# Kernel tuning notes

Hardware: AMD Instinct MI355X
Metric: run time of the kernel (lower is better)

The kernel has to match this reference:

```python
import jax, jax.numpy as jnp
import numpy as np
from jax import lax

DIM = 192
HEADS = 8
B, H, W = 8, 128, 128


def dwconv3x3(x, w):
    # x: [B,C,H,W], w: [C,1,3,3] depthwise (groups=C)
    return lax.conv_general_dilated(
        x, w, window_strides=(1, 1), padding='SAME',
        feature_group_count=x.shape[1],
        dimension_numbers=('NCHW', 'OIHW', 'NCHW'))


def conv1x1(x, w, b=None):
    # w: [Cout, Cin]
    y = jnp.einsum('oc,bchw->bohw', w, x)
    if b is not None:
        y = y + b[None, :, None, None]
    return y


def setup_inputs() -> dict:
    key = jax.random.key(0)
    ks = jax.random.split(key, 9)
    s = 0.02
    return {
        'x': jax.random.normal(ks[0], (B, DIM, H, W), jnp.float32),
        'w_qkv': jax.random.normal(ks[1], (3 * DIM, DIM), jnp.float32) * s,
        'b_qkv': jnp.zeros((3 * DIM,), jnp.float32),
        'w_dw': jax.random.normal(ks[2], (3 * DIM, 1, 3, 3), jnp.float32) * s,
        'b_dw': jnp.zeros((3 * DIM,), jnp.float32),
        'w_proj': jax.random.normal(ks[3], (DIM, DIM), jnp.float32) * s,
        'b_proj': jnp.zeros((DIM,), jnp.float32),
        'w_pos1': jax.random.normal(ks[4], (DIM, 1, 3, 3), jnp.float32) * s,
        'w_pos2': jax.random.normal(ks[5], (DIM, 1, 3, 3), jnp.float32) * s,
        'temperature': jnp.ones((HEADS, 1, 1), jnp.float32),
    }


def reference(x, w_qkv, b_qkv, w_dw, b_dw, w_proj, b_proj, w_pos1, w_pos2, temperature):
    b, c, h, w = x.shape
    heads = HEADS
    ch = c // heads

    qkv = conv1x1(x, w_qkv, b_qkv)
    qkv = dwconv3x3(qkv, w_dw) + b_dw[None, :, None, None]
    q_inp, k_inp, v_inp = jnp.split(qkv, 3, axis=1)

    def to_heads(t):  # [B,C,H,W] -> [B,heads,ch,HW]
        return t.reshape(b, heads, ch, h * w)

    q = to_heads(q_inp)
    k = to_heads(k_inp)
    v = to_heads(v_inp)

    # L2 normalize over hw (torch F.normalize, eps=1e-12)
    q = q / jnp.maximum(jnp.linalg.norm(q, axis=-1, keepdims=True), 1e-12)
    k = k / jnp.maximum(jnp.linalg.norm(k, axis=-1, keepdims=True), 1e-12)

    attn = jnp.einsum('bhce,bhde->bhcd', q, k) * temperature  # [B,heads,ch,ch]
    attn = jax.nn.softmax(attn, axis=-1)
    out = jnp.einsum('bhcd,bhde->bhce', attn, v)  # [B,heads,ch,HW]
    out = out.reshape(b, c, h, w)

    out = conv1x1(out, w_proj, b_proj)

    pos = dwconv3x3(v_inp, w_pos1)
    pos = jax.nn.gelu(pos, approximate=False)
    pos = dwconv3x3(pos, w_pos2)

    return out + pos
```

## Files before the change

### kernel.cpp

```cpp
#include <hip/hip_runtime.h>
#include <stdint.h>
#include <stddef.h>

#define NB 8
#define CC 192
#define C3 576
#define HGT 128
#define WID 128
#define HW 16384
#define NH 8
#define QKROW 49152

typedef short bf16x8 __attribute__((ext_vector_type(8)));
typedef float f32x4 __attribute__((ext_vector_type(4)));

__device__ __forceinline__ unsigned short f2bf(float f) {
  unsigned int u = __float_as_uint(f);
  u += 0x7fffu + ((u >> 16) & 1u);
  return (unsigned short)(u >> 16);
}
__device__ __forceinline__ float bf2f(unsigned short h) {
  return __uint_as_float(((unsigned int)h) << 16);
}
__device__ __forceinline__ float bflo(unsigned int v) {
  return __uint_as_float(v << 16);
}
__device__ __forceinline__ float bfhi(unsigned int v) {
  return __uint_as_float(v & 0xffff0000u);
}
__device__ __forceinline__ unsigned int pk2(float a, float b) {
  return (unsigned int)f2bf(a) | ((unsigned int)f2bf(b) << 16);
}
__device__ __forceinline__ void gl_lds16(const void* g, void* l) {
  __builtin_amdgcn_global_load_lds(
      (const __attribute__((address_space(1))) unsigned int*)(uintptr_t)g,
      (__attribute__((address_space(3))) unsigned int*)(uint32_t)(uintptr_t)l,
      16, 0, 0);
}
__device__ __forceinline__ int xcd_swz(int g, int n) {
  return (g & 7) * (n >> 3) + (g >> 3);
}

__global__ void kwprep(const float* __restrict__ wq, unsigned char* __restrict__ wb,
                       unsigned char* __restrict__ zero_region) {
  int f = blockIdx.x * 256 + threadIdx.x;
  if (f < 9984) *(uint4*)(zero_region + (size_t)f * 16) = (uint4){0, 0, 0, 0};
  if (f >= C3 * 24) return;
  int oc = f / 24, s = f % 24;
  unsigned int wv[4];
#pragma unroll
  for (int j = 0; j < 4; ++j)
    wv[j] = pk2(wq[oc * 192 + s * 8 + 2 * j], wq[oc * 192 + s * 8 + 2 * j + 1]);
  uint4 st; st.x = wv[0]; st.y = wv[1]; st.z = wv[2]; st.w = wv[3];
  *(uint4*)(wb + (size_t)oc * 384 + ((s ^ (oc & 7)) * 16)) = st;
}

__global__ __launch_bounds__(256) void kqkv(const float* __restrict__ x,
                                            const unsigned char* __restrict__ wb,
                                            const float* __restrict__ bqkv,
                                            unsigned short* __restrict__ vout,
                                            unsigned char* __restrict__ qkout) {
  __shared__ __align__(16) unsigned char lds[53248];
  const int ABF = 0;
  const int BB  = 24576;
  const int TR  = 49152;
  int wg = xcd_swz(blockIdx.x, gridDim.x);
  int t = wg & 255, b = wg >> 8;
  int p0 = t * 64;
  int tid = threadIdx.x;
  const unsigned char* gx = (const unsigned char*)(x + (size_t)b * CC * HW + p0);

  int p = tid & 63, sg = tid >> 6;
#pragma unroll
  for (int ck = 0; ck < 2; ++ck) {
#pragma unroll
    for (int i = 0; i < 6; ++i) {
      int f = i * 256 + tid;
      int ch = ck * 96 + (f >> 4), seg = f & 15;
      gl_lds16(gx + ((size_t)ch * HW + seg * 4) * 4, lds + BB + f * 16);
    }
    asm volatile("s_waitcnt vmcnt(0)" ::: "memory");
    __syncthreads();
    const float* lx = (const float*)(lds + BB);
#pragma unroll
    for (int s3 = 0; s3 < 3; ++s3) {
      int s = sg * 3 + s3;
      unsigned int wv[4];
#pragma unroll
      for (int j = 0; j < 4; ++j)
        wv[j] = pk2(lx[(s * 8 + 2 * j) * 64 + p], lx[(s * 8 + 2 * j + 1) * 64 + p]);
      uint4 st; st.x = wv[0]; st.y = wv[1]; st.z = wv[2]; st.w = wv[3];
      *(uint4*)(lds + ABF + ((ck * 12 + s) * 64 + p) * 16) = st;
    }
    __syncthreads();
  }
#pragma unroll
  for (int i = 0; i < 3; ++i)
    gl_lds16(wb + i * 4096 + tid * 16, lds + BB + i * 4096 + tid * 16);

  int lane = tid & 63, w = tid >> 6;
  int l15 = lane & 15, gq = lane >> 4;
  int pw = w * 16;
  int y = t >> 1, xh = (t & 1) * 8;
  int unitw = w * 2 + (gq >> 1);
  int sub8 = (gq & 1) * 8;
  int s4 = w * 4 + gq;
  int tc = tid & 31, tu = tid >> 5;
  int vcv = tid >> 3, vx = tid & 7;

  for (int j = 0; j < 18; ++j) {
    int ot = j >> 1, hh = j & 1, cur = j & 1;
    if (j == 0) { asm volatile("s_waitcnt vmcnt(0)" ::: "memory"); }
    else        { asm volatile("s_waitcnt vmcnt(1)" ::: "memory"); }
    __builtin_amdgcn_s_barrier();
    __builtin_amdgcn_sched_barrier(0);
    float bias0 = bqkv[ot * 64 + hh * 32 + l15];
    float bias1 = bqkv[ot * 64 + hh * 32 + 16 + l15];
    if (j < 17) {
      int jn = j + 1;
      const unsigned char* gB = wb + (size_t)(jn >> 1) * 24576 + (jn & 1) * 12288;
#pragma unroll
      for (int i = 0; i < 3; ++i)
        gl_lds16(gB + i * 4096 + tid * 16, lds + BB + (cur ^ 1) * 12288 + i * 4096 + tid * 16);
    }
    f32x4 acc[2];
    acc[0] = (f32x4){0.f, 0.f, 0.f, 0.f};
    acc[1] = (f32x4){0.f, 0.f, 0.f, 0.f};
#pragma unroll
    for (int kk = 0; kk < 6; ++kk) {
      bf16x8 a = *(const bf16x8*)(lds + ABF + (((kk * 4 + gq) * 64) + pw + l15) * 16);
      int cb = kk * 64 + gq * 16;
#pragma unroll
      for (int nf2 = 0; nf2 < 2; ++nf2) {
        int r2 = nf2 * 16 + l15;
        bf16x8 bfr = *(const bf16x8*)(lds + BB + cur * 12288 + r2 * 384 + (cb ^ ((r2 & 7) << 4)));
        acc[nf2] = __builtin_amdgcn_mfma_f32_16x16x32_bf16(a, bfr, acc[nf2], 0, 0, 0);
      }
    }
    bool isq = (ot < 6);
    if (isq) {
#pragma unroll
      for (int nf2 = 0; nf2 < 2; ++nf2) {
        int c = nf2 * 16 + l15;
        float bs = nf2 ? bias1 : bias0;
        uint2 st;
        st.x = pk2(acc[nf2][0] + bs, acc[nf2][1] + bs);
        st.y = pk2(acc[nf2][2] + bs, acc[nf2][3] + bs);
        *(uint2*)(lds + TR + c * 128 + ((unitw ^ (c & 7)) * 16) + sub8) = st;
      }
    } else {
#pragma unroll
      for (int nf2 = 0; nf2 < 2; ++nf2) {
        int c = nf2 * 16 + l15;
        float bs = nf2 ? bias1 : bias0;
        uint2 st;
        st.x = pk2(acc[nf2][0] + bs, acc[nf2][1] + bs);
        st.y = pk2(acc[nf2][2] + bs, acc[nf2][3] + bs);
        *(uint2*)(lds + TR + c * 128 + ((s4 ^ (c & 15)) * 8)) = st;
      }
    }
    asm volatile("s_waitcnt lgkmcnt(0)" ::: "memory");
    __builtin_amdgcn_s_barrier();
    __builtin_amdgcn_sched_barrier(0);
    if (isq) {
      int part = ot / 3, cm = (ot % 3) * 64 + hh * 32 + tc;
      uint4 v0 = *(const uint4*)(lds + TR + tc * 128 + ((tu ^ (tc & 7)) * 16));
      *(uint4*)(qkout + ((size_t)((part * 8 + b) * 128 + y)) * QKROW +
                (xh + tu) * 3072 + cm * 16) = v0;
    } else {
      uint2 q0 = *(const uint2*)(lds + TR + vcv * 128 + (((2 * vx) ^ (vcv & 15)) * 8));
      uint2 q1 = *(const uint2*)(lds + TR + vcv * 128 + (((2 * vx + 1) ^ (vcv & 15)) * 8));
      uint4 s0; s0.x = q0.x; s0.y = q0.y; s0.z = q1.x; s0.w = q1.y;
      *(uint4*)(vout + ((size_t)(b * CC + (ot - 6) * 64 + hh * 32 + vcv)) * HW +
                p0 + vx * 8) = s0;
    }
  }
}

__global__ __launch_bounds__(256) void kqk(const unsigned char* __restrict__ qk,
                                           const float* __restrict__ wdw,
                                           const float* __restrict__ bdw,
                                           float* __restrict__ G,
                                           float* __restrict__ nq,
                                           float* __restrict__ nk) {
  __shared__ __align__(16) unsigned char lds[49168];
  const int FB = 0;
  const int ZP = 24576;
  const int STG = 24592;
  int wg = xcd_swz(blockIdx.x, gridDim.x);
  int band = wg & 63, h = (wg >> 6) & 7, b = wg >> 9;
  int y0 = band * 2;
  int tid = threadIdx.x;
  if (tid == 0) *(uint4*)(lds + ZP) = (uint4){0, 0, 0, 0};

  int lane = tid & 63, w = tid >> 6;
  int ch = tid >> 3, row = (tid >> 2) & 1, qt = tid & 3;
  int u0 = qt * 4;

#pragma unroll
  for (int p = 0; p < 2; ++p) {
#pragma unroll
    for (int i = 0; i < 6; ++i) {
      int f = i * 256 + tid;
      int r = f / 384, unit = f % 384;
      int uc = unit / 24, cs = unit % 24;
      int yy = y0 - 1 + r;
      if (yy >= 0 && yy < HGT)
        gl_lds16(qk + ((size_t)((p * 8 + b) * 128 + yy)) * QKROW + uc * 3072 + (h * 24 + cs) * 16,
                 lds + STG + f * 16);
      else
        *(uint4*)(lds + STG + f * 16) = (uint4){0, 0, 0, 0};
    }
    asm volatile("s_waitcnt vmcnt(0)" ::: "memory");
    __syncthreads();
    if (tid < 192) {
      int gc = p * 192 + h * 24 + ch;
      float wv[9];
#pragma unroll
      for (int j = 0; j < 9; ++j) wv[j] = wdw[gc * 9 + j];
      float bias = bdw[gc];
      const unsigned char* sbase = lds + STG + ch * 16;
      unsigned char* fb = lds + FB + p * 12288 + (row * 4 + qt) * 1536 + ch * 16;
      unsigned int W[3][16];
#define LOADU3(dy_, m_, u_) { \
    uint4 tt = ((u_) >= 0 && (u_) < 16) \
        ? *(const uint4*)(sbase + (row + (dy_)) * 6144 + (u_) * 384) \
        : (uint4){0, 0, 0, 0}; \
    W[dy_][(m_) * 4 + 0] = tt.x; W[dy_][(m_) * 4 + 1] = tt.y; \
    W[dy_][(m_) * 4 + 2] = tt.z; W[dy_][(m_) * 4 + 3] = tt.w; }
#pragma unroll
      for (int dy = 0; dy < 3; ++dy) {
#pragma unroll
        for (int m = 0; m < 4; ++m) { LOADU3(dy, m, u0 - 1 + m); }
      }
      float nsum = 0.f;
#pragma unroll
      for (int c4 = 0; c4 < 2; ++c4) {
        if (c4 > 0) {
#pragma unroll
          for (int dy = 0; dy < 3; ++dy) {
#pragma unroll
            for (int e = 0; e < 8; ++e) W[dy][e] = W[dy][8 + e];
            LOADU3(dy, 2, u0 + 3);
            LOADU3(dy, 3, u0 + 4);
          }
        }
        float acc[16];
#pragma unroll
        for (int j = 0; j < 16; ++j) acc[j] = bias;
#pragma unroll
        for (int dy = 0; dy < 3; ++dy) {
          float f[18];
#pragma unroll
          for (int t2 = 0; t2 < 18; ++t2) {
            int rel = 7 + t2;
            unsigned int v = W[dy][rel >> 1];
            f[t2] = (rel & 1) ? bfhi(v) : bflo(v);
          }
#pragma unroll
          for (int j = 0; j < 16; ++j)
            acc[j] += f[j] * wv[dy * 3] + f[j + 1] * wv[dy * 3 + 1] + f[j + 2] * wv[dy * 3 + 2];
        }
#pragma unroll
        for (int j = 0; j < 16; ++j) nsum += acc[j] * acc[j];
        unsigned int pk[8];
#pragma unroll
        for (int e = 0; e < 8; ++e) pk[e] = pk2(acc[2 * e], acc[2 * e + 1]);
        uint4 s0; s0.x = pk[0]; s0.y = pk[1]; s0.z = pk[2]; s0.w = pk[3];
        uint4 s1; s1.x = pk[4]; s1.y = pk[5]; s1.z = pk[6]; s1.w = pk[7];
        *(uint4*)(fb + (c4 * 2) * 384) = s0;
        *(uint4*)(fb + (c4 * 2 + 1) * 384) = s1;
      }
#undef LOADU3
      nsum += __shfl_xor(nsum, 1);
      nsum += __shfl_xor(nsum, 2);
      nsum += __shfl_xor(nsum, 4);
      if ((tid & 7) == 0) {
        float* dst = (p == 0) ? nq : nk;
        atomicAdd(dst + (b * NH + h) * 24 + ch, nsum);
      }
    }
    __syncthreads();
  }

  int l15 = lane & 15, gq = lane >> 4;
  f32x4 acc2[2][2];
#pragma unroll
  for (int ct = 0; ct < 2; ++ct)
#pragma unroll
    for (int dt = 0; dt < 2; ++dt) acc2[ct][dt] = (f32x4){0.f, 0.f, 0.f, 0.f};
#pragma unroll
  for (int t2 = 0; t2 < 2; ++t2) {
    int kt = w * 2 + t2;
    bf16x8 aq[2], bk[2];
#pragma unroll
    for (int ct = 0; ct < 2; ++ct) {
      int c = ct * 16 + l15;
      const unsigned char* qa =
          (c < 24) ? (lds + FB + kt * 1536 + gq * 384 + c * 16) : (lds + ZP);
      const unsigned char* ka =
          (c < 24) ? (lds + FB + 12288 + kt * 1536 + gq * 384 + c * 16) : (lds + ZP);
      aq[ct] = *(const bf16x8*)qa;
      bk[ct] = *(const bf16x8*)ka;
    }
#pragma unroll
    for (int ct = 0; ct < 2; ++ct)
#pragma unroll
      for (int dt = 0; dt < 2; ++dt)
        acc2[ct][dt] = __builtin_amdgcn_mfma_f32_16x16x32_bf16(aq[ct], bk[dt], acc2[ct][dt], 0, 0, 0);
  }
  float* gp = (float*)(lds + STG);
#pragma unroll
  for (int ct = 0; ct < 2; ++ct)
#pragma unroll
    for (int dt = 0; dt < 2; ++dt)
      *(f32x4*)(gp + (((w * 4 + ct * 2 + dt) * 64) + lane) * 4) = acc2[ct][dt];
  __syncthreads();
  float* Gb = G + (size_t)(b * NH + h) * 576;
#pragma unroll
  for (int ii = 0; ii < 3; ++ii) {
    int f = ii * 256 + tid;
    if (f < 576) {
      int c = f / 24, d = f % 24;
      int t4 = ((c >> 4) << 1) + (d >> 4);
      int lane16 = (d & 15) + (((c & 15) >> 2) << 4);
      int reg = c & 3;
      float s = 0.f;
#pragma unroll
      for (int w4 = 0; w4 < 4; ++w4)
        s += gp[((w4 * 4 + t4) * 64 + lane16) * 4 + reg];
      atomicAdd(Gb + f, s);
    }
  }
}

__global__ __launch_bounds__(256) void kdwv(const unsigned short* __restrict__ src,
                                            const float* __restrict__ wdw,
                                            const float* __restrict__ bdw,
                                            unsigned char* __restrict__ vT) {
  __shared__ __align__(16) unsigned int smem[8 * 721];
  int wg = xcd_swz(blockIdx.x, gridDim.x);
  int cg = wg % 24, rt = (wg / 24) & 15, b = wg / 384;
  int y0 = rt * 8, chg0 = cg * 8;
  int tid = threadIdx.x;
  for (int i = tid; i < 5768; i += 256) smem[i] = 0;
  __syncthreads();
#pragma unroll
  for (int i = 0; i < 5; ++i) {
    int f = i * 256 + tid;
    int ch = f / 160, rem = f % 160;
    int r = rem >> 4, seg = rem & 15;
    int y = y0 - 1 + r;
    if (y >= 0 && y < HGT) {
      uint4 v = *(const uint4*)(src + ((size_t)(b * CC + chg0 + ch)) * HW + y * WID + seg * 8);
      unsigned int* dp = smem + ch * 721 + r * 72 + 4 + seg * 4;
      dp[0] = v.x; dp[1] = v.y; dp[2] = v.z; dp[3] = v.w;
    }
  }
  __syncthreads();
  int ch = tid >> 5, u = tid & 31;
  int row = u >> 2, xs = (u & 3) * 32;
  int gch = 384 + chg0 + ch;
  float wv[9];
#pragma unroll
  for (int j = 0; j < 9; ++j) wv[j] = wdw[gch * 9 + j];
  float bias = bdw[gch];
  float outv[32];
  const unsigned int* tb = smem + ch * 721;
#pragma unroll
  for (int g = 0; g < 4; ++g) {
    int x0 = xs + g * 8;
    float v[3][12];
#pragma unroll
    for (int dy = 0; dy < 3; ++dy) {
      const unsigned int* rp = tb + (row + dy) * 72 + ((x0 + 6) >> 1);
#pragma unroll
      for (int m = 0; m < 6; ++m) {
        unsigned int w2 = rp[m];
        v[dy][2 * m] = bf2f((unsigned short)(w2 & 0xffff));
        v[dy][2 * m + 1] = bf2f((unsigned short)(w2 >> 16));
      }
    }
#pragma unroll
    for (int j = 0; j < 8; ++j) {
      float a = bias;
#pragma unroll
      for (int dy = 0; dy < 3; ++dy)
#pragma unroll
        for (int dx = 0; dx < 3; ++dx)
          a += v[dy][j + dx + 1] * wv[dy * 3 + dx];
      outv[g * 8 + j] = a;
    }
  }
  __syncthreads();
  unsigned short* vt = (unsigned short*)smem;
#pragma unroll
  for (int g = 0; g < 4; ++g)
#pragma unroll
    for (int j = 0; j < 8; j += 2) {
      int x = xs + g * 8 + j;
      ((unsigned int*)smem)[ch * 512 + row * 64 + (x >> 1)] =
          pk2(outv[g * 8 + j], outv[g * 8 + j + 1]);
    }
  __syncthreads();
#pragma unroll
  for (int i = 0; i < 4; ++i) {
    int f = i * 256 + tid;
    int r = f >> 7, col = f & 127;
    unsigned int wvp[4];
#pragma unroll
    for (int e = 0; e < 4; ++e) {
      unsigned short a = vt[(2 * e) * 1024 + r * 128 + col];
      unsigned short bb = vt[(2 * e + 1) * 1024 + r * 128 + col];
      wvp[e] = (unsigned int)a | ((unsigned int)bb << 16);
    }
    uint4 st; st.x = wvp[0]; st.y = wvp[1]; st.z = wvp[2]; st.w = wvp[3];
    *(uint4*)(vT + (((size_t)(b * 24 + cg)) * HW + (size_t)(y0 + r) * WID + col) * 16) = st;
  }
}

__global__ __launch_bounds__(256) void kattn(const float* __restrict__ G,
                                             const float* __restrict__ nq,
                                             const float* __restrict__ nk,
                                             const float* __restrict__ temp,
                                             const float* __restrict__ wproj,
                                             unsigned char* __restrict__ W2) {
  __shared__ float attn[24][24];
  __shared__ float iq[24], ik[24];
  int bh = blockIdx.x;
  int h = bh & 7, b = bh >> 3;
  int tid = threadIdx.x;
  const float* Gb = G + (size_t)bh * 576;
  if (tid < 24) { float n = sqrtf(nq[bh * 24 + tid]); iq[tid] = 1.f / fmaxf(n, 1e-12f); }
  else if (tid < 48) { float n = sqrtf(nk[bh * 24 + tid - 24]); ik[tid - 24] = 1.f / fmaxf(n, 1e-12f); }
  __syncthreads();
  if (tid < 24) {
    float tmp = temp[h];
    float row[24];
    float mx = -1e30f;
#pragma unroll
    for (int d = 0; d < 24; ++d) {
      row[d] = Gb[tid * 24 + d] * iq[tid] * ik[d] * tmp;
      mx = fmaxf(mx, row[d]);
    }
    float sum = 0.f;
#pragma unroll
    for (int d = 0; d < 24; ++d) { float e = expf(row[d] - mx); row[d] = e; sum += e; }
    float inv = 1.f / sum;
#pragma unroll
    for (int d = 0; d < 24; ++d) attn[tid][d] = row[d] * inv;
  }
  __syncthreads();
  for (int i = 0; i < 18; ++i) {
    int f = tid + i * 256;
    if (f >= 4608) break;
    int oc = f / 24, d = f % 24;
    float s = 0.f;
#pragma unroll
    for (int c = 0; c < 24; ++c) s += wproj[oc * 192 + h * 24 + c] * attn[c][d];
    int gg = h * 24 + d;
    *(unsigned short*)(W2 + ((size_t)b * CC + oc) * 384 + ((gg * 2) ^ ((oc & 7) << 4))) = f2bf(s);
  }
}

__global__ __launch_bounds__(256) void kpos(const unsigned char* __restrict__ vT,
                                            const float* __restrict__ w1,
                                            const float* __restrict__ w2,
                                            unsigned short* __restrict__ pos) {
  __shared__ unsigned int vbuf[8 * 865];
  __shared__ unsigned int d1[8 * 721];
  int wg = xcd_swz(blockIdx.x, gridDim.x);
  int cg = wg % 24, rt = (wg / 24) & 15, b = wg / 384;
  int y0 = rt * 8, g0 = cg * 8;
  int tid = threadIdx.x;
  for (int i = tid; i < 6920; i += 256) vbuf[i] = 0;
  __syncthreads();
#pragma unroll
  for (int i = 0; i < 3; ++i) {
    int f = i * 256 + tid;
    int r = f >> 6, colp = f & 63;
    int y = y0 - 2 + r;
    if (y >= 0 && y < HGT) {
      const unsigned char* base = vT + (((size_t)(b * 24 + cg)) * HW + (size_t)y * WID + colp * 2) * 16;
      uint4 va = *(const uint4*)(base);
      uint4 vb2 = *(const uint4*)(base + 16);
      unsigned int la[4] = {va.x, va.y, va.z, va.w};
      unsigned int lb[4] = {vb2.x, vb2.y, vb2.z, vb2.w};
#pragma unroll
      for (int e = 0; e < 8; ++e) {
        unsigned int a16 = (la[e >> 1] >> ((e & 1) * 16)) & 0xffff;
        unsigned int b16 = (lb[e >> 1] >> ((e & 1) * 16)) & 0xffff;
        vbuf[e * 865 + r * 72 + colp + 4] = a16 | (b16 << 16);
      }
    }
  }
  __syncthreads();
  int ch = tid >> 5, u = tid & 31;
  {
    const float* wp = w1 + (g0 + ch) * 9;
    float wl[9];
#pragma unroll
    for (int j = 0; j < 9; ++j) wl[j] = wp[j];
    int x0 = u * 4;
    for (int rr = 0; rr < 10; ++rr) {
      int y = y0 - 1 + rr;
      unsigned int o0 = 0, o1 = 0;
      if (y >= 0 && y < HGT) {
        float v[3][8];
#pragma unroll
        for (int dy = 0; dy < 3; ++dy) {
          const unsigned int* rp = vbuf + ch * 865 + (rr + dy) * 72 + ((x0 + 6) >> 1);
#pragma unroll
          for (int m = 0; m < 4; ++m) {
            unsigned int w2r = rp[m];
            v[dy][2 * m] = bf2f((unsigned short)(w2r & 0xffff));
            v[dy][2 * m + 1] = bf2f((unsigned short)(w2r >> 16));
          }
        }
        float g4[4];
#pragma unroll
        for (int j = 0; j < 4; ++j) {
          float a = 0.f;
#pragma unroll
          for (int dy = 0; dy < 3; ++dy)
#pragma unroll
            for (int dx = 0; dx < 3; ++dx)
              a += v[dy][j + dx + 1] * wl[dy * 3 + dx];
          g4[j] = 0.5f * a * (1.f + erff(a * 0.70710678118f));
        }
        o0 = pk2(g4[0], g4[1]);
        o1 = pk2(g4[2], g4[3]);
      }
      unsigned int* dp = d1 + ch * 721 + rr * 72 + ((x0 + 8) >> 1);
      dp[0] = o0; dp[1] = o1;
    }
  }
  if (tid < 160) {
    int ech = tid / 20, rem = tid % 20;
    int rr = rem >> 1, side = rem & 1;
    int x = side ? 128 : -1;
    int y = y0 - 1 + rr;
    unsigned short val = 0;
    if (y >= 0 && y < HGT) {
      const float* wp = w1 + (g0 + ech) * 9;
      float a = 0.f;
      const unsigned short* vb16 = (const unsigned short*)(vbuf + ech * 865);
#pragma unroll
      for (int dy = 0; dy < 3; ++dy)
#pragma unroll
        for (int dx = 0; dx < 3; ++dx)
          a += bf2f(vb16[(rr + dy) * 144 + (x + dx + 7)]) * wp[dy * 3 + dx];
      val = f2bf(0.5f * a * (1.f + erff(a * 0.70710678118f)));
    }
    ((unsigned short*)(d1 + ech * 721))[rr * 144 + (x + 8)] = val;
  }
  __syncthreads();
  {
    const float* wp = w2 + (g0 + ch) * 9;
    float wl[9];
#pragma unroll
    for (int j = 0; j < 9; ++j) wl[j] = wp[j];
    int row = u >> 2, xs = (u & 3) * 32;
    size_t rb = ((size_t)(b * CC + g0 + ch)) * HW + (size_t)(y0 + row) * WID;
#pragma unroll
    for (int g = 0; g < 4; ++g) {
      int x0 = xs + g * 8;
      float v[3][12];
#pragma unroll
      for (int dy = 0; dy < 3; ++dy) {
        const unsigned int* rp = d1 + ch * 721 + (row + dy) * 72 + ((x0 + 6) >> 1);
#pragma unroll
        for (int m = 0; m < 6; ++m) {
          unsigned int w2r = rp[m];
          v[dy][2 * m] = bf2f((unsigned short)(w2r & 0xffff));
          v[dy][2 * m + 1] = bf2f((unsigned short)(w2r >> 16));
        }
      }
      uint4 st;
      float o[8];
#pragma unroll
      for (int j = 0; j < 8; ++j) {
        float a = 0.f;
#pragma unroll
        for (int dy = 0; dy < 3; ++dy)
#pragma unroll
          for (int dx = 0; dx < 3; ++dx)
            a += v[dy][j + dx + 1] * wl[dy * 3 + dx];
        o[j] = a;
      }
      st.x = pk2(o[0], o[1]); st.y = pk2(o[2], o[3]);
      st.z = pk2(o[4], o[5]); st.w = pk2(o[6], o[7]);
      *(uint4*)(pos + rb + x0) = st;
    }
  }
}

__global__ __launch_bounds__(256) void kproj(const unsigned char* __restrict__ vT,
                                             const unsigned char* __restrict__ W2,
                                             const float* __restrict__ bproj,
                                             const unsigned short* __restrict__ pos,
                                             float* __restrict__ out) {
  __shared__ __align__(16) unsigned char lds[73728];
  int wg = xcd_swz(blockIdx.x, gridDim.x);
  int ot = wg % 3; int rest = wg / 3; int grp = rest & 63; int b = rest >> 6;
  int tid = threadIdx.x;
  const unsigned char* gB = W2 + ((size_t)(b * 192 + ot * 64)) * 384;
#pragma unroll
  for (int i = 0; i < 6; ++i)
    gl_lds16(gB + i * 4096 + tid * 16, lds + 49152 + i * 4096 + tid * 16);
  const unsigned char* gA = vT + (size_t)b * 24 * HW * 16;
  int t0 = grp * 4;
  {
    int p0 = t0 * 64;
#pragma unroll
    for (int i = 0; i < 6; ++i) {
      int f = i * 256 + tid;
      gl_lds16(gA + (((size_t)(f >> 6)) * HW + p0 + (f & 63)) * 16, lds + f * 16);
    }
  }
  int lane = tid & 63, w = tid >> 6;
  int l15 = lane & 15, gq = lane >> 4;
  int pw = w * 16;
  float bias[4];
  size_t obase[4];
#pragma unroll
  for (int nf = 0; nf < 4; ++nf) {
    int oc = ot * 64 + nf * 16 + l15;
    bias[nf] = bproj[oc];
    obase[nf] = ((size_t)(b * 192 + oc)) * HW;
  }
  for (int it = 0; it < 4; ++it) {
    int tile = t0 + it;
    if (it == 0) { asm volatile("s_waitcnt vmcnt(0)" ::: "memory"); }
    else         { asm volatile("s_waitcnt vmcnt(4)" ::: "memory"); }
    __builtin_amdgcn_s_barrier();
    __builtin_amdgcn_sched_barrier(0);
    int nb = it & 1;
    int p = tile * 64 + pw + gq * 4;
    uint2 pv[4];
#pragma unroll
    for (int nf = 0; nf < 4; ++nf)
      pv[nf] = *(const uint2*)(pos + obase[nf] + p);
    if (it < 3) {
      int p1 = (tile + 1) * 64;
#pragma unroll
      for (int i = 0; i < 6; ++i) {
        int f = i * 256 + tid;
        gl_lds16(gA + (((size_t)(f >> 6)) * HW + p1 + (f & 63)) * 16,
                 lds + ((nb ^ 1) * 24576) + f * 16);
      }
    }
    __builtin_amdgcn_sched_barrier(0);
    f32x4 acc[4];
#pragma unroll
    for (int nf = 0; nf < 4; ++nf) acc[nf] = (f32x4){0.f, 0.f, 0.f, 0.f};
#pragma unroll
    for (int kk = 0; kk < 6; ++kk) {
      bf16x8 a = *(const bf16x8*)(lds + nb * 24576 + ((((kk * 4 + gq) << 6) + pw + l15) * 16));
      int cb = kk * 64 + gq * 16;
#pragma unroll
      for (int nf = 0; nf < 4; ++nf) {
        int r = nf * 16 + l15;
        bf16x8 bfr = *(const bf16x8*)(lds + 49152 + r * 384 + (cb ^ ((r & 7) << 4)));
        acc[nf] = __builtin_amdgcn_mfma_f32_16x16x32_bf16(a, bfr, acc[nf], 0, 0, 0);
      }
    }
#pragma unroll
    for (int nf = 0; nf < 4; ++nf) {
      float4 o;
      o.x = acc[nf][0] + bias[nf] + bf2f((unsigned short)(pv[nf].x & 0xffff));
      o.y = acc[nf][1] + bias[nf] + bf2f((unsigned short)(pv[nf].x >> 16));
      o.z = acc[nf][2] + bias[nf] + bf2f((unsigned short)(pv[nf].y & 0xffff));
      o.w = acc[nf][3] + bias[nf] + bf2f((unsigned short)(pv[nf].y >> 16));
      *(float4*)(out + obase[nf] + p) = o;
    }
  }
}

#define OFF_W   ((size_t)0)
#define OFF_G   ((size_t)221184)
#define OFF_NQ  ((size_t)368640)
#define OFF_NK  ((size_t)374784)
#define OFF_W2  ((size_t)380928)
#define OFF_QK  ((size_t)970752)
#define OFF_V   ((size_t)101634048)
#define OFF_XT  ((size_t)151965696)

extern "C" void kernel_launch(void* const* d_in, const int* in_sizes, int n_in,
                              void* d_out, int out_size, void* d_ws, size_t ws_size,
                              hipStream_t stream) {
  const float* x     = (const float*)d_in[0];
  const float* wqkv  = (const float*)d_in[1];
  const float* bqkv  = (const float*)d_in[2];
  const float* wdw   = (const float*)d_in[3];
  const float* bdw   = (const float*)d_in[4];
  const float* wproj = (const float*)d_in[5];
  const float* bproj = (const float*)d_in[6];
  const float* wpos1 = (const float*)d_in[7];
  const float* wpos2 = (const float*)d_in[8];
  const float* temp  = (const float*)d_in[9];
  unsigned char* ws = (unsigned char*)d_ws;

  kwprep<<<54, 256, 0, stream>>>(wqkv, ws + OFF_W, ws + OFF_G);
  kqkv<<<2048, 256, 0, stream>>>(x, ws + OFF_W, bqkv,
                                 (unsigned short*)(ws + OFF_V), ws + OFF_QK);
  kqk<<<4096, 256, 0, stream>>>(ws + OFF_QK, wdw, bdw, (float*)(ws + OFF_G),
                                (float*)(ws + OFF_NQ), (float*)(ws + OFF_NK));
  kdwv<<<3072, 256, 0, stream>>>((const unsigned short*)(ws + OFF_V), wdw, bdw,
                                 ws + OFF_XT);
  kattn<<<64, 256, 0, stream>>>((const float*)(ws + OFF_G), (const float*)(ws + OFF_NQ),
                                (const float*)(ws + OFF_NK), temp, wproj, ws + OFF_W2);
  kpos<<<3072, 256, 0, stream>>>(ws + OFF_XT, wpos1, wpos2,
                                 (unsigned short*)(ws + OFF_QK));
  kproj<<<1536, 256, 0, stream>>>(ws + OFF_XT, ws + OFF_W2, bproj,
                                  (const unsigned short*)(ws + OFF_QK), (float*)d_out);
}
```

Before: 285.6 us.

## Store QK projection directly to global in 4-pixel units, skipping LDS transpose

The QKV projection kernel now writes Q/K tiles straight from MFMA accumulators to global memory in a new layout of 4-pixel-by-channel 8-byte chunks. This removes the LDS transpose stage, its barrier and its lgkmcnt wait for the Q/K outputs. The consumer kernel's gather and LDS reads are rewritten to match, now using two 8-byte LDS loads instead of one 16-byte load. The direct writes are smaller (8 bytes per lane) and less coalesced, and the vmcnt wait counts are adjusted to account for the extra outstanding stores.

Result: slower. 299.2 us (+4.8%).

```diff
diff --git a/kernel.cpp b/kernel.cpp
--- a/kernel.cpp
+++ b/kernel.cpp
@@ -9,7 +9,7 @@
 #define WID 128
 #define HW 16384
 #define NH 8
-#define QKROW 49152
+#define QKPL ((size_t)6291456)
 
 typedef short bf16x8 __attribute__((ext_vector_type(8)));
 typedef float f32x4 __attribute__((ext_vector_type(4)));
@@ -101,17 +101,15 @@
   int lane = tid & 63, w = tid >> 6;
   int l15 = lane & 15, gq = lane >> 4;
   int pw = w * 16;
-  int y = t >> 1, xh = (t & 1) * 8;
-  int unitw = w * 2 + (gq >> 1);
-  int sub8 = (gq & 1) * 8;
   int s4 = w * 4 + gq;
-  int tc = tid & 31, tu = tid >> 5;
   int vcv = tid >> 3, vx = tid & 7;
+  size_t u4base = (size_t)(t * 16 + w * 4 + gq) * 1536;
 
   for (int j = 0; j < 18; ++j) {
     int ot = j >> 1, hh = j & 1, cur = j & 1;
-    if (j == 0) { asm volatile("s_waitcnt vmcnt(0)" ::: "memory"); }
-    else        { asm volatile("s_waitcnt vmcnt(1)" ::: "memory"); }
+    if (j == 0)       { asm volatile("s_waitcnt vmcnt(0)" ::: "memory"); }
+    else if (j <= 12) { asm volatile("s_waitcnt vmcnt(2)" ::: "memory"); }
+    else              { asm volatile("s_waitcnt vmcnt(1)" ::: "memory"); }
     __builtin_amdgcn_s_barrier();
     __builtin_amdgcn_sched_barrier(0);
     float bias0 = bqkv[ot * 64 + hh * 32 + l15];
@@ -123,6 +121,7 @@
       for (int i = 0; i < 3; ++i)
         gl_lds16(gB + i * 4096 + tid * 16, lds + BB + (cur ^ 1) * 12288 + i * 4096 + tid * 16);
     }
+    __builtin_amdgcn_sched_barrier(0);
     f32x4 acc[2];
     acc[0] = (f32x4){0.f, 0.f, 0.f, 0.f};
     acc[1] = (f32x4){0.f, 0.f, 0.f, 0.f};
@@ -139,14 +138,16 @@
     }
     bool isq = (ot < 6);
     if (isq) {
+      int part = ot / 3, cm0 = (ot % 3) * 64 + hh * 32;
+      unsigned char* gout = qkout + (size_t)(part * 8 + b) * QKPL + u4base;
 #pragma unroll
       for (int nf2 = 0; nf2 < 2; ++nf2) {
-        int c = nf2 * 16 + l15;
+        int cm = cm0 + nf2 * 16 + l15;
         float bs = nf2 ? bias1 : bias0;
         uint2 st;
         st.x = pk2(acc[nf2][0] + bs, acc[nf2][1] + bs);
         st.y = pk2(acc[nf2][2] + bs, acc[nf2][3] + bs);
-        *(uint2*)(lds + TR + c * 128 + ((unitw ^ (c & 7)) * 16) + sub8) = st;
+        *(uint2*)(gout + cm * 8) = st;
       }
     } else {
 #pragma unroll
@@ -158,16 +159,9 @@
         st.y = pk2(acc[nf2][2] + bs, acc[nf2][3] + bs);
         *(uint2*)(lds + TR + c * 128 + ((s4 ^ (c & 15)) * 8)) = st;
       }
-    }
-    asm volatile("s_waitcnt lgkmcnt(0)" ::: "memory");
-    __builtin_amdgcn_s_barrier();
-    __builtin_amdgcn_sched_barrier(0);
-    if (isq) {
-      int part = ot / 3, cm = (ot % 3) * 64 + hh * 32 + tc;
-      uint4 v0 = *(const uint4*)(lds + TR + tc * 128 + ((tu ^ (tc & 7)) * 16));
-      *(uint4*)(qkout + ((size_t)((part * 8 + b) * 128 + y)) * QKROW +
-                (xh + tu) * 3072 + cm * 16) = v0;
-    } else {
+      asm volatile("s_waitcnt lgkmcnt(0)" ::: "memory");
+      __builtin_amdgcn_s_barrier();
+      __builtin_amdgcn_sched_barrier(0);
       uint2 q0 = *(const uint2*)(lds + TR + vcv * 128 + (((2 * vx) ^ (vcv & 15)) * 8));
       uint2 q1 = *(const uint2*)(lds + TR + vcv * 128 + (((2 * vx + 1) ^ (vcv & 15)) * 8));
       uint4 s0; s0.x = q0.x; s0.y = q0.y; s0.z = q1.x; s0.w = q1.y;
@@ -203,10 +197,11 @@
     for (int i = 0; i < 6; ++i) {
       int f = i * 256 + tid;
       int r = f / 384, unit = f % 384;
-      int uc = unit / 24, cs = unit % 24;
+      int u4 = unit / 12, cp = unit % 12;
       int yy = y0 - 1 + r;
       if (yy >= 0 && yy < HGT)
-        gl_lds16(qk + ((size_t)((p * 8 + b) * 128 + yy)) * QKROW + uc * 3072 + (h * 24 + cs) * 16,
+        gl_lds16(qk + (size_t)(p * 8 + b) * QKPL +
+                 (size_t)(yy * 32 + u4) * 1536 + (h * 24 + cp * 2) * 8,
                  lds + STG + f * 16);
       else
         *(uint4*)(lds + STG + f * 16) = (uint4){0, 0, 0, 0};
@@ -219,15 +214,18 @@
 #pragma unroll
       for (int j = 0; j < 9; ++j) wv[j] = wdw[gc * 9 + j];
       float bias = bdw[gc];
-      const unsigned char* sbase = lds + STG + ch * 16;
+      const unsigned char* sb2 = lds + STG + (ch >> 1) * 16 + (ch & 1) * 8;
       unsigned char* fb = lds + FB + p * 12288 + (row * 4 + qt) * 1536 + ch * 16;
       unsigned int W[3][16];
 #define LOADU3(dy_, m_, u_) { \
-    uint4 tt = ((u_) >= 0 && (u_) < 16) \
-        ? *(const uint4*)(sbase + (row + (dy_)) * 6144 + (u_) * 384) \
-        : (uint4){0, 0, 0, 0}; \
-    W[dy_][(m_) * 4 + 0] = tt.x; W[dy_][(m_) * 4 + 1] = tt.y; \
-    W[dy_][(m_) * 4 + 2] = tt.z; W[dy_][(m_) * 4 + 3] = tt.w; }
+    uint2 ta, tb; \
+    if ((u_) >= 0 && (u_) < 16) { \
+      const unsigned char* ap = sb2 + (row + (dy_)) * 6144 + (2 * (u_)) * 192; \
+      ta = *(const uint2*)(ap); \
+      tb = *(const uint2*)(ap + 192); \
+    } else { ta = (uint2){0, 0}; tb = (uint2){0, 0}; } \
+    W[dy_][(m_) * 4 + 0] = ta.x; W[dy_][(m_) * 4 + 1] = ta.y; \
+    W[dy_][(m_) * 4 + 2] = tb.x; W[dy_][(m_) * 4 + 3] = tb.y; }
 #pragma unroll
       for (int dy = 0; dy < 3; ++dy) {
 #pragma unroll
```
